# Kernel optimization log

Measured on AMD Instinct MI355X. Metric: run time of the kernel, lower is better.

Reference implementation:

```python
import jax, jax.numpy as jnp
import numpy as np

FILTER_K = 10      # per-class top-K support retention
TAU = 1.0          # temperature
SCALE = 20.0       # prototype logit scale
EPS = 1e-12


def _normalize(x, axis=-1):
    n = jnp.linalg.norm(x, axis=axis, keepdims=True)
    return x / jnp.maximum(n, EPS)


def _entropy(logits):
    p = jax.nn.softmax(logits, axis=1)
    return -(p * jax.nn.log_softmax(logits, axis=1)).sum(axis=1)


def _quantile(x, q):
    # linear-interpolation quantile (matches torch.quantile default)
    s = jnp.sort(x)
    n = x.shape[0]
    pos = q * (n - 1)
    lo = jnp.floor(pos).astype(jnp.int32)
    hi = jnp.minimum(lo + 1, n - 1)
    frac = pos - lo.astype(x.dtype)
    return s[lo] * (1.0 - frac) + s[hi] * frac


def setup_inputs() -> dict:
    key = jax.random.key(0)
    k1, k2, k3, k4, k5 = jax.random.split(key, 5)
    B, D, C = 65536, 512, 50
    feat = jax.random.normal(k1, (B, D), jnp.float32)
    logits_raw = jax.random.normal(k2, (B, C), jnp.float32)
    logits_aug = jax.random.normal(k3, (B, C), jnp.float32)
    W = jax.random.normal(k4, (C, D), jnp.float32) * 0.05  # classifier weight
    b = jax.random.normal(k5, (C,), jnp.float32) * 0.05    # classifier bias
    return {"feat": feat, "logits_raw": logits_raw, "logits_aug": logits_aug, "W": W, "b": b}


def reference(feat, logits_raw, logits_aug, W, b):
    C, D = W.shape
    # --- warmup memory initialized from classifier weights (as in __init__) ---
    wl = W @ W.T + b                       # (C, C)
    p0 = jax.nn.softmax(wl, axis=1)
    lab0 = jnp.argmax(wl, axis=1)          # (C,)
    ent0 = _entropy(wl)
    conf0 = p0.max(axis=1)

    # --- online batch stats ---
    logits = feat @ W.T + b                # (B, C)
    p = jax.nn.softmax(logits, axis=1)
    yhat = jnp.argmax(logits, axis=1)
    ent = _entropy(logits)
    pmax = p.max(axis=1)

    # dynamic entropy-quantile threshold (ent_thresh=None path)
    m = ent.mean()
    dyn_q = jnp.where(m >= 0.45, 0.25, jnp.where(m >= 0.38, 0.3, 0.4))
    thr = _quantile(ent, dyn_q)
    mask = ent <= thr
    # dual-view consistency gate
    mask &= jnp.argmax(logits_raw, axis=1) == jnp.argmax(logits_aug, axis=1)
    # confidence gate
    conf_thr = jnp.where(m >= 0.45, 0.72, 0.62)
    mask &= pmax >= conf_thr

    # --- grown support memory (warmup + accepted batch samples), static shape + valid mask ---
    supports = jnp.concatenate([W, feat], axis=0)          # (C+B, D)
    lab_idx = jnp.concatenate([lab0, yhat], axis=0)        # (C+B,)
    ents = jnp.concatenate([ent0, ent], axis=0)
    conf = jnp.concatenate([conf0, pmax], axis=0)
    valid = jnp.concatenate([jnp.ones((C,), bool), mask], axis=0)

    # --- per-class top-K lowest-entropy pruning (vectorized over classes) ---
    cls_mask = (lab_idx[None, :] == jnp.arange(C)[:, None]) & valid[None, :]  # (C, C+B)
    masked_ent = jnp.where(cls_mask, ents[None, :], jnp.inf)
    order = jnp.argsort(masked_ent, axis=1)
    ranks = jnp.argsort(order, axis=1)                     # rank of each entry within its class
    keep = (cls_mask & (ranks < FILTER_K)).any(axis=0)     # (C+B,)

    # --- confidence-weighted centroids + cosine-sim classification ---
    S = _normalize(supports)
    onehot = jax.nn.one_hot(lab_idx, C, dtype=supports.dtype)
    lab_w = onehot * jnp.maximum(conf, 1e-6)[:, None] * keep[:, None].astype(supports.dtype)
    denom = jnp.maximum(lab_w.sum(axis=0, keepdims=True), EPS)
    centroids = _normalize((lab_w / denom).T @ S)          # (C, D)
    sim = _normalize(feat) @ centroids.T                   # (B, C)
    return SCALE * sim / max(TAU, 1e-6)
```

## Files before the change

kernel.cpp:

```cpp
#include <hip/hip_runtime.h>
#include <math.h>

constexpr int BN = 65536;
constexpr int DK = 512;
constexpr int CN = 50;
constexpr int FILTK = 10;
constexpr int MB = 64;
constexpr int SELB = 64;
constexpr int CAP = 6144;
constexpr int ASTR = 132;

typedef __attribute__((ext_vector_type(8))) short short8;
typedef __attribute__((ext_vector_type(4))) float f4;

constexpr int W_SC     = 0;
constexpr int W_H1     = 64;
constexpr int W_H2LO   = 2112;
constexpr int W_H2HI   = 4160;
constexpr int W_H3LO   = 6208;
constexpr int W_H3HI   = 7232;
constexpr int ZERO_WORDS = 8256;
constexpr int W_WFH    = 8256;
constexpr int W_WFL    = W_WFH + 16384;
constexpr int W_CFH    = W_WFL + 16384;
constexpr int W_CFL    = W_CFH + 16384;
constexpr int W_ENT    = W_CFL + 16384;
constexpr int W_PMAX   = W_ENT  + BN;
constexpr int W_YHAT   = W_PMAX + BN;
constexpr int W_CONS   = W_YHAT + BN;
constexpr int W_NORM   = W_CONS + BN;
constexpr int W_LAB0   = W_NORM + BN;
constexpr int W_ENT0   = W_LAB0 + 64;
constexpr int W_CONF0  = W_ENT0 + 64;
constexpr int W_WNORM  = W_CONF0 + 64;
constexpr int LE_CAP   = BN + 64;
constexpr int W_LECLS  = W_WNORM + 64;
constexpr int W_LEENT  = W_LECLS  + LE_CAP;
constexpr int W_LECONF = W_LEENT  + LE_CAP;
constexpr int W_LEORD  = W_LECONF + LE_CAP;
constexpr int W_LESRC  = W_LEORD  + LE_CAP;

struct Scalars {
    float    sum_ent;
    float    mean;
    float    conf_thr;
    float    frac;
    int      klo;
    int      khi;
    unsigned prefix_lo;
    unsigned rank_lo;
    unsigned prefix_hi;
    unsigned rank_hi;
    float    thr;
    unsigned cnt;
    unsigned done1, done2, done3;
};

__device__ __forceinline__ unsigned fkey(float f) {
    unsigned u = __float_as_uint(f);
    return (u & 0x80000000u) ? ~u : (u | 0x80000000u);
}
__device__ __forceinline__ float funkey(unsigned u) {
    return (u & 0x80000000u) ? __uint_as_float(u & 0x7fffffffu) : __uint_as_float(~u);
}

__device__ __forceinline__ short bf16h(float x) {
    unsigned u = __float_as_uint(x);
    return (short)((u + 0x7fffu + ((u >> 16) & 1u)) >> 16);
}
__device__ __forceinline__ float bf16tof(short h) {
    return __uint_as_float(((unsigned)(unsigned short)h) << 16);
}
__device__ __forceinline__ void cvt8(const float* a, short8& h, short8& l) {
    #pragma unroll
    for (int j = 0; j < 8; j++) {
        short hh = bf16h(a[j]);
        h[j] = hh;
        l[j] = bf16h(a[j] - bf16tof(hh));
    }
}
__device__ __forceinline__ int fragidx(int ks, int n, int q, int j) {
    return ks * 2048 + (n >> 4) * 512 + ((n & 15) + 16 * q) * 8 + j;
}

__global__ void init_kernel(const float* __restrict__ W, const float* __restrict__ bias,
                            int* __restrict__ lab0, float* __restrict__ ent0,
                            float* __restrict__ conf0, float* __restrict__ wnorm,
                            unsigned* __restrict__ wsz,
                            short* __restrict__ wfh, short* __restrict__ wfl) {
    const int b = blockIdx.x, l = threadIdx.x;
    if (b >= 64) {
        for (int i = (b - 64) * 64 + l; i < ZERO_WORDS; i += 128) wsz[i] = 0u;
        return;
    }
    {
        int ks = l >> 2, q = l & 3;
        int dst = fragidx(ks, b, q, 0);
        if (b < CN) {
            const float* wp = W + b * DK + l * 8;
            f4 x = *(const f4*)wp, y = *(const f4*)(wp + 4);
            float a8[8] = {x[0], x[1], x[2], x[3], y[0], y[1], y[2], y[3]};
            short8 h, lo2; cvt8(a8, h, lo2);
            *(short8*)(wfh + dst) = h;
            *(short8*)(wfl + dst) = lo2;
        } else {
            short8 z;
            #pragma unroll
            for (int j = 0; j < 8; j++) z[j] = 0;
            *(short8*)(wfh + dst) = z;
            *(short8*)(wfl + dst) = z;
        }
    }
    if (b >= CN) return;

    __shared__ float wrow[DK];
    const int i = b;
    f4 v0 = *(const f4*)(W + i * DK + l * 4);
    f4 v1 = *(const f4*)(W + i * DK + 256 + l * 4);
    *(f4*)(wrow + l * 4) = v0;
    *(f4*)(wrow + 256 + l * 4) = v1;
    float sq = v0[0]*v0[0] + v0[1]*v0[1] + v0[2]*v0[2] + v0[3]*v0[3]
             + v1[0]*v1[0] + v1[1]*v1[1] + v1[2]*v1[2] + v1[3]*v1[3];
    #pragma unroll
    for (int m = 1; m < 64; m <<= 1) sq += __shfl_xor(sq, m);
    if (l == 0) wnorm[i] = sqrtf(sq);
    __syncthreads();

    float dot = -INFINITY;
    int   ai  = 0x7fffffff;
    if (l < CN) {
        const float* wj = W + l * DK;
        float d2 = 0.f;
        for (int d = 0; d < DK; d += 4) {
            f4 a = *(const f4*)(wrow + d);
            f4 b4 = *(const f4*)(wj + d);
            d2 = fmaf(a[0], b4[0], fmaf(a[1], b4[1], fmaf(a[2], b4[2], fmaf(a[3], b4[3], d2))));
        }
        dot = d2 + bias[l];
        ai  = l;
    }
    float mx = dot; int am = ai;
    #pragma unroll
    for (int m = 32; m >= 1; m >>= 1) {
        float o = __shfl_xor(mx, m); int oi = __shfl_xor(am, m);
        if (o > mx || (o == mx && oi < am)) { mx = o; am = oi; }
    }
    float e = 0.f, te = 0.f;
    if (l < CN) { e = expf(dot - mx); te = e * (dot - mx); }
    #pragma unroll
    for (int m = 1; m < 64; m <<= 1) { e += __shfl_xor(e, m); te += __shfl_xor(te, m); }
    if (l == 0) {
        lab0[i]  = am;
        ent0[i]  = logf(e) - te / e;
        conf0[i] = 1.f / e;
    }
}

template <int MODE>
__global__ __launch_bounds__(256) void gemm_kernel(
        const float* __restrict__ feat,
        const short* __restrict__ bfh, const short* __restrict__ bfl,
        const float* __restrict__ bias,
        float* __restrict__ ent, float* __restrict__ pmaxA,
        int* __restrict__ yhat, float* __restrict__ rnorm,
        const float* __restrict__ lraw, const float* __restrict__ laug,
        unsigned* __restrict__ consp, Scalars* sc, float* __restrict__ outp) {
    __shared__ float As[MB * ASTR];
    const int t = threadIdx.x;
    const int w = t >> 6, lane = t & 63, m = lane & 15, q = lane >> 4;
    const int rb = blockIdx.x * MB;
    const float* fbase = feat + (size_t)rb * DK;

    f4 acc[4];
    #pragma unroll
    for (int nt = 0; nt < 4; nt++) acc[nt] = (f4){0.f, 0.f, 0.f, 0.f};
    float sq = 0.f;

    const int scol = (t & 31) * 4;
    const int srow0 = t >> 5;

    for (int kc = 0; kc < 4; kc++) {
        if (kc) __syncthreads();
        #pragma unroll
        for (int r8 = 0; r8 < 8; r8++) {
            int row = r8 * 8 + srow0;
            f4 v = *(const f4*)(fbase + (size_t)row * DK + kc * 128 + scol);
            *(f4*)(&As[row * ASTR + scol]) = v;
        }
        __syncthreads();
        #pragma unroll
        for (int ks = 0; ks < 4; ks++) {
            const float* ap = &As[(w * 16 + m) * ASTR + ks * 32 + q * 8];
            f4 x = *(const f4*)ap;
            f4 y = *(const f4*)(ap + 4);
            float a8[8] = {x[0], x[1], x[2], x[3], y[0], y[1], y[2], y[3]};
            if (MODE == 0) {
                sq += x[0]*x[0] + x[1]*x[1] + x[2]*x[2] + x[3]*x[3]
                    + y[0]*y[0] + y[1]*y[1] + y[2]*y[2] + y[3]*y[3];
            }
            short8 ah, al;
            cvt8(a8, ah, al);
            const int ksg = kc * 4 + ks;
            short8 bh[4], bl[4];
            #pragma unroll
            for (int nt = 0; nt < 4; nt++) {
                int off = ksg * 2048 + nt * 512 + lane * 8;
                bh[nt] = *(const short8*)(bfh + off);
                bl[nt] = *(const short8*)(bfl + off);
            }
            #pragma unroll
            for (int nt = 0; nt < 4; nt++) {
                acc[nt] = __builtin_amdgcn_mfma_f32_16x16x32_bf16(ah, bh[nt], acc[nt], 0, 0, 0);
                acc[nt] = __builtin_amdgcn_mfma_f32_16x16x32_bf16(al, bh[nt], acc[nt], 0, 0, 0);
                acc[nt] = __builtin_amdgcn_mfma_f32_16x16x32_bf16(ah, bl[nt], acc[nt], 0, 0, 0);
            }
        }
    }

    if (MODE == 0) {
        float s = sq;
        s += __shfl_xor(s, 16);
        s += __shfl_xor(s, 32);
        if (q == 0) rnorm[rb + w * 16 + m] = sqrtf(s);
        __syncthreads();
        float* L = As;
        float bc[4];
        #pragma unroll
        for (int nt = 0; nt < 4; nt++) { int c = nt * 16 + m; bc[nt] = (c < CN) ? bias[c] : 0.f; }
        #pragma unroll
        for (int nt = 0; nt < 4; nt++)
            #pragma unroll
            for (int r = 0; r < 4; r++) {
                int row = w * 16 + q * 4 + r;
                L[row * 65 + nt * 16 + m] = acc[nt][r] + bc[nt];
            }
        __syncthreads();
        if (t < MB) {
            int grow = rb + t;
            const float* Lr = L + t * 65;
            float mx = Lr[0]; int am = 0;
            #pragma unroll 10
            for (int j = 1; j < CN; j++) { float v = Lr[j]; if (v > mx) { mx = v; am = j; } }
            float ssum = 0.f, tt = 0.f;
            for (int j = 0; j < CN; j++) {
                float d = Lr[j] - mx;
                float e = expf(d);
                ssum += e; tt += e * d;
            }
            float ev = logf(ssum) - tt / ssum;
            ent  [grow] = ev;
            pmaxA[grow] = 1.f / ssum;
            yhat [grow] = am;
            const float* rp  = lraw + (size_t)grow * CN;
            const float* apg = laug + (size_t)grow * CN;
            float m1 = rp[0];  int a1 = 0;
            float m2 = apg[0]; int a2 = 0;
            #pragma unroll 10
            for (int j = 1; j < CN; j++) {
                float v1 = rp[j];  if (v1 > m1) { m1 = v1; a1 = j; }
                float v2 = apg[j]; if (v2 > m2) { m2 = v2; a2 = j; }
            }
            consp[grow] = (a1 == a2) ? 1u : 0u;
            float es = ev;
            #pragma unroll
            for (int mk = 1; mk < 64; mk <<= 1) es += __shfl_xor(es, mk);
            if (t == 0) atomicAdd(&sc->sum_ent, es);
        }
    } else {
        #pragma unroll
        for (int r = 0; r < 4; r++) {
            int grow = rb + w * 16 + q * 4 + r;
            float s = 20.f / fmaxf(rnorm[grow], 1e-12f);
            #pragma unroll
            for (int nt = 0; nt < 4; nt++) {
                int c = nt * 16 + m;
                if (c < CN) outp[(size_t)grow * CN + c] = acc[nt][r] * s;
            }
        }
    }
}

__global__ __launch_bounds__(256) void sel1_kernel(const float* __restrict__ ent,
                                                   unsigned* __restrict__ H1, Scalars* sc) {
    __shared__ unsigned h[2048];
    __shared__ unsigned part[256];
    __shared__ int last;
    const int t = threadIdx.x;
    for (int b = t; b < 2048; b += 256) h[b] = 0u;
    __syncthreads();
    const int lo = blockIdx.x * (BN / SELB), hi = lo + (BN / SELB);
    for (int i = lo + t; i < hi; i += 256)
        atomicAdd(&h[fkey(ent[i]) >> 21], 1u);
    __syncthreads();
    for (int b = t; b < 2048; b += 256) if (h[b]) atomicAdd(&H1[b], h[b]);
    __threadfence();
    if (t == 0) last = (atomicAdd(&sc->done1, 1u) == SELB - 1) ? 1 : 0;
    __syncthreads();
    if (!last) return;

    for (int b = t; b < 2048; b += 256) h[b] = atomicAdd(&H1[b], 0u);
    __syncthreads();
    unsigned ps = 0;
    #pragma unroll
    for (int j = 0; j < 8; j++) ps += h[t * 8 + j];
    part[t] = ps;
    __syncthreads();
    if (t == 0) {
        float m = sc->sum_ent / (float)BN;
        sc->mean = m;
        float q = (m >= 0.45f) ? 0.25f : ((m >= 0.38f) ? 0.30f : 0.40f);
        sc->conf_thr = (m >= 0.45f) ? 0.72f : 0.62f;
        float pos = q * (float)(BN - 1);
        float flo = floorf(pos);
        sc->frac = pos - flo;
        int klo = (int)flo;
        int khi = klo + 1; if (khi > BN - 1) khi = BN - 1;
        sc->klo = klo; sc->khi = khi;
        for (int pass = 0; pass < 2; pass++) {
            unsigned k = (pass == 0) ? (unsigned)klo : (unsigned)khi;
            unsigned cum = 0; int c = 0;
            for (; c < 255; c++) { unsigned pc = part[c]; if (cum + pc > k) break; cum += pc; }
            int b = c * 8;
            for (; b < c * 8 + 7; b++) { unsigned hb = h[b]; if (cum + hb > k) break; cum += hb; }
            if (pass == 0) { sc->prefix_lo = (unsigned)b; sc->rank_lo = k - cum; }
            else           { sc->prefix_hi = (unsigned)b; sc->rank_hi = k - cum; }
        }
    }
}

__global__ __launch_bounds__(256) void sel2_kernel(const float* __restrict__ ent,
                                                   unsigned* __restrict__ HLO, unsigned* __restrict__ HHI,
                                                   Scalars* sc) {
    __shared__ unsigned hlo[2048], hhi[2048];
    __shared__ unsigned plo_s[256], phi_s[256];
    __shared__ int last;
    const int t = threadIdx.x;
    const unsigned plo = sc->prefix_lo, phi = sc->prefix_hi;
    for (int b = t; b < 2048; b += 256) { hlo[b] = 0u; hhi[b] = 0u; }
    __syncthreads();
    const int lo = blockIdx.x * (BN / SELB), hi = lo + (BN / SELB);
    for (int i = lo + t; i < hi; i += 256) {
        unsigned u = fkey(ent[i]);
        unsigned d1 = u >> 21, d2 = (u >> 10) & 2047u;
        if (d1 == plo) atomicAdd(&hlo[d2], 1u);
        if (d1 == phi) atomicAdd(&hhi[d2], 1u);
    }
    __syncthreads();
    for (int b = t; b < 2048; b += 256) {
        if (hlo[b]) atomicAdd(&HLO[b], hlo[b]);
        if (hhi[b]) atomicAdd(&HHI[b], hhi[b]);
    }
    __threadfence();
    if (t == 0) last = (atomicAdd(&sc->done2, 1u) == SELB - 1) ? 1 : 0;
    __syncthreads();
    if (!last) return;

    for (int b = t; b < 2048; b += 256) { hlo[b] = atomicAdd(&HLO[b], 0u); hhi[b] = atomicAdd(&HHI[b], 0u); }
    __syncthreads();
    unsigned pl = 0, ph = 0;
    #pragma unroll
    for (int j = 0; j < 8; j++) { pl += hlo[t * 8 + j]; ph += hhi[t * 8 + j]; }
    plo_s[t] = pl; phi_s[t] = ph;
    __syncthreads();
    if (t == 0) {
        {
            unsigned k = sc->rank_lo, cum = 0; int c = 0;
            for (; c < 255; c++) { unsigned pc = plo_s[c]; if (cum + pc > k) break; cum += pc; }
            int b = c * 8;
            for (; b < c * 8 + 7; b++) { unsigned hb = hlo[b]; if (cum + hb > k) break; cum += hb; }
            sc->prefix_lo = (plo << 11) | (unsigned)b; sc->rank_lo = k - cum;
        }
        {
            unsigned k = sc->rank_hi, cum = 0; int c = 0;
            for (; c < 255; c++) { unsigned pc = phi_s[c]; if (cum + pc > k) break; cum += pc; }
            int b = c * 8;
            for (; b < c * 8 + 7; b++) { unsigned hb = hhi[b]; if (cum + hb > k) break; cum += hb; }
            sc->prefix_hi = (phi << 11) | (unsigned)b; sc->rank_hi = k - cum;
        }
    }
}

__global__ __launch_bounds__(256) void sel3_kernel(const float* __restrict__ ent,
                                                   unsigned* __restrict__ HLO, unsigned* __restrict__ HHI,
                                                   Scalars* sc) {
    __shared__ unsigned hlo[1024], hhi[1024];
    __shared__ unsigned plo_s[256], phi_s[256];
    __shared__ int last;
    const int t = threadIdx.x;
    const unsigned plo = sc->prefix_lo, phi = sc->prefix_hi;
    for (int b = t; b < 1024; b += 256) { hlo[b] = 0u; hhi[b] = 0u; }
    __syncthreads();
    const int lo = blockIdx.x * (BN / SELB), hi = lo + (BN / SELB);
    for (int i = lo + t; i < hi; i += 256) {
        unsigned u = fkey(ent[i]);
        unsigned p22 = u >> 10, d3 = u & 1023u;
        if (p22 == plo) atomicAdd(&hlo[d3], 1u);
        if (p22 == phi) atomicAdd(&hhi[d3], 1u);
    }
    __syncthreads();
    for (int b = t; b < 1024; b += 256) {
        if (hlo[b]) atomicAdd(&HLO[b], hlo[b]);
        if (hhi[b]) atomicAdd(&HHI[b], hhi[b]);
    }
    __threadfence();
    if (t == 0) last = (atomicAdd(&sc->done3, 1u) == SELB - 1) ? 1 : 0;
    __syncthreads();
    if (!last) return;

    for (int b = t; b < 1024; b += 256) { hlo[b] = atomicAdd(&HLO[b], 0u); hhi[b] = atomicAdd(&HHI[b], 0u); }
    __syncthreads();
    unsigned pl = 0, ph = 0;
    #pragma unroll
    for (int j = 0; j < 4; j++) { pl += hlo[t * 4 + j]; ph += hhi[t * 4 + j]; }
    plo_s[t] = pl; phi_s[t] = ph;
    __syncthreads();
    if (t == 0) {
        float vlo, vhi;
        {
            unsigned k = sc->rank_lo, cum = 0; int c = 0;
            for (; c < 255; c++) { unsigned pc = plo_s[c]; if (cum + pc > k) break; cum += pc; }
            int b = c * 4;
            for (; b < c * 4 + 3; b++) { unsigned hb = hlo[b]; if (cum + hb > k) break; cum += hb; }
            vlo = funkey((plo << 10) | (unsigned)b);
        }
        {
            unsigned k = sc->rank_hi, cum = 0; int c = 0;
            for (; c < 255; c++) { unsigned pc = phi_s[c]; if (cum + pc > k) break; cum += pc; }
            int b = c * 4;
            for (; b < c * 4 + 3; b++) { unsigned hb = hhi[b]; if (cum + hb > k) break; cum += hb; }
            vhi = funkey((phi << 10) | (unsigned)b);
        }
        sc->thr = vlo * (1.f - sc->frac) + vhi * sc->frac;
    }
}

__global__ __launch_bounds__(256) void compact_kernel(
        const float* __restrict__ ent, const float* __restrict__ pmaxA,
        const int* __restrict__ yhat, const unsigned* __restrict__ cons,
        const int* __restrict__ lab0, const float* __restrict__ ent0,
        const float* __restrict__ conf0, Scalars* sc,
        int* le_cls, float* le_ent, float* le_conf, int* le_ord, int* le_src) {
    int i = blockIdx.x * blockDim.x + threadIdx.x;
    if (i < CN) {
        le_cls[i] = lab0[i]; le_ent[i] = ent0[i]; le_conf[i] = conf0[i];
        le_ord[i] = i; le_src[i] = i;
    }
    if (i >= BN) return;
    bool m = (ent[i] <= sc->thr) && (cons[i] != 0u) && (pmaxA[i] >= sc->conf_thr);
    if (m) {
        int pos = (int)atomicAdd(&sc->cnt, 1u);
        int e = CN + pos;
        le_cls[e] = yhat[i]; le_ent[e] = ent[i]; le_conf[e] = pmaxA[i];
        le_ord[e] = CN + i;  le_src[e] = i;
    }
}

__global__ __launch_bounds__(256) void tail2_kernel(
        const Scalars* sc, const int* __restrict__ le_cls,
        const float* __restrict__ le_ent, const float* __restrict__ le_conf,
        const int* __restrict__ le_ord, const int* __restrict__ le_src,
        const float* __restrict__ W, const float* __restrict__ feat,
        const float* __restrict__ wnorm, const float* __restrict__ rnorm,
        short* __restrict__ cfh, short* __restrict__ cfl) {
    const int c = blockIdx.x, t = threadIdx.x;
    if (c >= CN) {
        for (int idx = t; idx < 512; idx += 256) {
            int ks = idx >> 5, rem = idx & 31, qq = rem >> 3, jj = rem & 7;
            int dst = fragidx(ks, c, qq, jj);
            cfh[dst] = 0; cfl[dst] = 0;
        }
        return;
    }
    __shared__ float sent[CAP];
    __shared__ int   sord[CAP];
    __shared__ float sconf[CAP];
    __shared__ int   ssrc[CAP];
    __shared__ float wk[CAP];
    __shared__ float accv[DK];
    __shared__ float red[4];
    __shared__ int   mc_s;
    if (t == 0) mc_s = 0;
    for (int d = t; d < DK; d += 256) accv[d] = 0.f;
    __syncthreads();
    const int M = CN + (int)sc->cnt;
    for (int e = t; e < M; e += 256) {
        if (le_cls[e] == c) {
            int i = atomicAdd(&mc_s, 1);
            if (i < CAP) { sent[i] = le_ent[e]; sord[i] = le_ord[e]; sconf[i] = le_conf[e]; ssrc[i] = le_src[e]; }
        }
    }
    __syncthreads();
    int mc = min(mc_s, CAP);
    for (int i = t; i < mc; i += 256) {
        float v = sent[i]; int o = sord[i]; int r = 0;
        for (int j = 0; j < mc && r < FILTK; j++)
            if (sent[j] < v || (sent[j] == v && sord[j] < o)) r++;
        wk[i] = (r < FILTK) ? fmaxf(sconf[i], 1e-6f) : 0.f;
    }
    __syncthreads();
    for (int i = 0; i < mc; i++) {
        float wgt = wk[i];
        if (wgt <= 0.f) continue;
        int src = ssrc[i];
        bool warm = sord[i] < CN;
        const float* rowp = warm ? (W + src * DK) : (feat + (size_t)src * DK);
        float nr = warm ? wnorm[src] : rnorm[src];
        float k = wgt / fmaxf(nr, 1e-12f);
        for (int d = t; d < DK; d += 256) accv[d] += k * rowp[d];
    }
    __syncthreads();
    float s = 0.f;
    for (int d = t; d < DK; d += 256) { float v = accv[d]; s = fmaf(v, v, s); }
    #pragma unroll
    for (int mk = 1; mk < 64; mk <<= 1) s += __shfl_xor(s, mk);
    if ((t & 63) == 0) red[t >> 6] = s;
    __syncthreads();
    float inv = 1.f / fmaxf(sqrtf(red[0] + red[1] + red[2] + red[3]), 1e-12f);
    for (int k = t; k < DK; k += 256) {
        float v = accv[k] * inv;
        short hh = bf16h(v);
        short ll = bf16h(v - bf16tof(hh));
        int ks = k >> 5, kk = k & 31, qq = kk >> 3, jj = kk & 7;
        int dst = fragidx(ks, c, qq, jj);
        cfh[dst] = hh; cfl[dst] = ll;
    }
}

extern "C" void kernel_launch(void* const* d_in, const int* in_sizes, int n_in,
                              void* d_out, int out_size, void* d_ws, size_t ws_size,
                              hipStream_t stream) {
    const float* feat = (const float*)d_in[0];
    const float* lraw = (const float*)d_in[1];
    const float* laug = (const float*)d_in[2];
    const float* W    = (const float*)d_in[3];
    const float* bias = (const float*)d_in[4];
    float* out = (float*)d_out;

    unsigned* wsw    = (unsigned*)d_ws;
    Scalars*  sc     = (Scalars*)(wsw + W_SC);
    unsigned* H1     = wsw + W_H1;
    unsigned* H2LO   = wsw + W_H2LO;
    unsigned* H2HI   = wsw + W_H2HI;
    unsigned* H3LO   = wsw + W_H3LO;
    unsigned* H3HI   = wsw + W_H3HI;
    short*    wfh    = (short*)(wsw + W_WFH);
    short*    wfl    = (short*)(wsw + W_WFL);
    short*    cfh    = (short*)(wsw + W_CFH);
    short*    cfl    = (short*)(wsw + W_CFL);
    float*    ent    = (float*)(wsw + W_ENT);
    float*    pmaxA  = (float*)(wsw + W_PMAX);
    int*      yhat   = (int*)(wsw + W_YHAT);
    unsigned* cons   = wsw + W_CONS;
    float*    rnorm  = (float*)(wsw + W_NORM);
    int*      lab0   = (int*)(wsw + W_LAB0);
    float*    ent0   = (float*)(wsw + W_ENT0);
    float*    conf0  = (float*)(wsw + W_CONF0);
    float*    wnorm  = (float*)(wsw + W_WNORM);
    int*      le_cls = (int*)(wsw + W_LECLS);
    float*    le_ent = (float*)(wsw + W_LEENT);
    float*    le_conf= (float*)(wsw + W_LECONF);
    int*      le_ord = (int*)(wsw + W_LEORD);
    int*      le_src = (int*)(wsw + W_LESRC);

    init_kernel<<<66, 64, 0, stream>>>(W, bias, lab0, ent0, conf0, wnorm, wsw, wfh, wfl);
    gemm_kernel<0><<<BN / MB, 256, 0, stream>>>(feat, wfh, wfl, bias, ent, pmaxA, yhat, rnorm,
                                                lraw, laug, cons, sc, nullptr);
    sel1_kernel<<<SELB, 256, 0, stream>>>(ent, H1, sc);
    sel2_kernel<<<SELB, 256, 0, stream>>>(ent, H2LO, H2HI, sc);
    sel3_kernel<<<SELB, 256, 0, stream>>>(ent, H3LO, H3HI, sc);
    compact_kernel<<<BN / 256, 256, 0, stream>>>(ent, pmaxA, yhat, cons, lab0, ent0, conf0, sc,
                                                 le_cls, le_ent, le_conf, le_ord, le_src);
    tail2_kernel<<<64, 256, 0, stream>>>(sc, le_cls, le_ent, le_conf, le_ord, le_src,
                                         W, feat, wnorm, rnorm, cfh, cfl);
    gemm_kernel<1><<<BN / MB, 256, 0, stream>>>(feat, cfh, cfl, nullptr, nullptr, nullptr, nullptr, rnorm,
                                                nullptr, nullptr, nullptr, sc, out);
}
```

Baseline: 357.5 us.

## Double-buffer per-wave LDS tiles in GEMM, drop block barriers, simplify bf16 split

Each wave now stages only its own 16 feature rows into a private double-buffered LDS region. The next k-chunk is prefetched into registers while the current chunk is consumed, which removes the block-wide __syncthreads between chunks. The B fragments for a whole k-chunk are also loaded up front. Separately, the bf16 hi/lo split switches from round-to-nearest-even to a simpler round-half-up, and launch bounds request 2 blocks per CU. The costs are much higher register pressure (bh/bl arrays of 32 short8 plus 8 staged f4), a larger LDS footprint, and slightly different rounding of the split.

```diff
diff --git a/kernel.cpp b/kernel.cpp
--- a/kernel.cpp
+++ b/kernel.cpp
@@ -8,7 +8,8 @@
 constexpr int MB = 64;
 constexpr int SELB = 64;
 constexpr int CAP = 6144;
-constexpr int ASTR = 132;
+constexpr int WSTR = 132;
+constexpr int WBUF = 16 * WSTR;
 
 typedef __attribute__((ext_vector_type(8))) short short8;
 typedef __attribute__((ext_vector_type(4))) float f4;
@@ -64,20 +65,21 @@
     return (u & 0x80000000u) ? __uint_as_float(u & 0x7fffffffu) : __uint_as_float(~u);
 }
 
+__device__ __forceinline__ void cvt8(const float* a, short8& h, short8& l) {
+    #pragma unroll
+    for (int j = 0; j < 8; j++) {
+        unsigned u = __float_as_uint(a[j]);
+        unsigned r = (u + 0x8000u) & 0xffff0000u;
+        float lo_f = a[j] - __uint_as_float(r);
+        h[j] = (short)(r >> 16);
+        l[j] = (short)((__float_as_uint(lo_f) + 0x8000u) >> 16);
+    }
+}
 __device__ __forceinline__ short bf16h(float x) {
-    unsigned u = __float_as_uint(x);
-    return (short)((u + 0x7fffu + ((u >> 16) & 1u)) >> 16);
+    return (short)((__float_as_uint(x) + 0x8000u) >> 16);
 }
 __device__ __forceinline__ float bf16tof(short h) {
     return __uint_as_float(((unsigned)(unsigned short)h) << 16);
-}
-__device__ __forceinline__ void cvt8(const float* a, short8& h, short8& l) {
-    #pragma unroll
-    for (int j = 0; j < 8; j++) {
-        short hh = bf16h(a[j]);
-        h[j] = hh;
-        l[j] = bf16h(a[j] - bf16tof(hh));
-    }
 }
 __device__ __forceinline__ int fragidx(int ks, int n, int q, int j) {
     return ks * 2048 + (n >> 4) * 512 + ((n & 15) + 16 * q) * 8 + j;
@@ -157,7 +159,7 @@
 }
 
 template <int MODE>
-__global__ __launch_bounds__(256) void gemm_kernel(
+__global__ __launch_bounds__(256, 2) void gemm_kernel(
         const float* __restrict__ feat,
         const short* __restrict__ bfh, const short* __restrict__ bfl,
         const float* __restrict__ bias,
@@ -165,55 +167,73 @@
         int* __restrict__ yhat, float* __restrict__ rnorm,
         const float* __restrict__ lraw, const float* __restrict__ laug,
         unsigned* __restrict__ consp, Scalars* sc, float* __restrict__ outp) {
-    __shared__ float As[MB * ASTR];
+    __shared__ float As[4 * 2 * WBUF];
     const int t = threadIdx.x;
     const int w = t >> 6, lane = t & 63, m = lane & 15, q = lane >> 4;
     const int rb = blockIdx.x * MB;
-    const float* fbase = feat + (size_t)rb * DK;
+    const int wr0 = rb + w * 16;
+    float* myLDS = As + w * (2 * WBUF);
+
+    const int sr  = lane >> 5;
+    const int sc4 = lane & 31;
 
     f4 acc[4];
     #pragma unroll
     for (int nt = 0; nt < 4; nt++) acc[nt] = (f4){0.f, 0.f, 0.f, 0.f};
     float sq = 0.f;
 
-    const int scol = (t & 31) * 4;
-    const int srow0 = t >> 5;
+    {
+        f4 stg[8];
+        #pragma unroll
+        for (int r8 = 0; r8 < 8; r8++)
+            stg[r8] = *(const f4*)(feat + (size_t)(wr0 + r8 * 2 + sr) * DK + sc4 * 4);
+        #pragma unroll
+        for (int r8 = 0; r8 < 8; r8++)
+            *(f4*)(myLDS + (r8 * 2 + sr) * WSTR + sc4 * 4) = stg[r8];
+    }
 
     for (int kc = 0; kc < 4; kc++) {
-        if (kc) __syncthreads();
-        #pragma unroll
-        for (int r8 = 0; r8 < 8; r8++) {
-            int row = r8 * 8 + srow0;
-            f4 v = *(const f4*)(fbase + (size_t)row * DK + kc * 128 + scol);
-            *(f4*)(&As[row * ASTR + scol]) = v;
-        }
-        __syncthreads();
+        const int cur = kc & 1;
+        short8 bh[4][4], bl[4][4];
         #pragma unroll
         for (int ks = 0; ks < 4; ks++) {
-            const float* ap = &As[(w * 16 + m) * ASTR + ks * 32 + q * 8];
+            const int ksg = kc * 4 + ks;
+            #pragma unroll
+            for (int nt = 0; nt < 4; nt++) {
+                const int off = ksg * 2048 + nt * 512 + lane * 8;
+                bh[ks][nt] = *(const short8*)(bfh + off);
+                bl[ks][nt] = *(const short8*)(bfl + off);
+            }
+        }
+        f4 stg[8];
+        if (kc < 3) {
+            #pragma unroll
+            for (int r8 = 0; r8 < 8; r8++)
+                stg[r8] = *(const f4*)(feat + (size_t)(wr0 + r8 * 2 + sr) * DK + (kc + 1) * 128 + sc4 * 4);
+        }
+        #pragma unroll
+        for (int ks = 0; ks < 4; ks++) {
+            const float* ap = myLDS + cur * WBUF + m * WSTR + ks * 32 + q * 8;
             f4 x = *(const f4*)ap;
             f4 y = *(const f4*)(ap + 4);
-            float a8[8] = {x[0], x[1], x[2], x[3], y[0], y[1], y[2], y[3]};
             if (MODE == 0) {
                 sq += x[0]*x[0] + x[1]*x[1] + x[2]*x[2] + x[3]*x[3]
                     + y[0]*y[0] + y[1]*y[1] + y[2]*y[2] + y[3]*y[3];
             }
+            float a8[8] = {x[0], x[1], x[2], x[3], y[0], y[1], y[2], y[3]};
             short8 ah, al;
             cvt8(a8, ah, al);
-            const int ksg = kc * 4 + ks;
-            short8 bh[4], bl[4];
             #pragma unroll
             for (int nt = 0; nt < 4; nt++) {
-                int off = ksg * 2048 + nt * 512 + lane * 8;
-                bh[nt] = *(const short8*)(bfh + off);
-                bl[nt] = *(const short8*)(bfl + off);
-            }
-            #pragma unroll
-            for (int nt = 0; nt < 4; nt++) {
-                acc[nt] = __builtin_amdgcn_mfma_f32_16x16x32_bf16(ah, bh[nt], acc[nt], 0, 0, 0);
-                acc[nt] = __builtin_amdgcn_mfma_f32_16x16x32_bf16(al, bh[nt], acc[nt], 0, 0, 0);
-                acc[nt] = __builtin_amdgcn_mfma_f32_16x16x32_bf16(ah, bl[nt], acc[nt], 0, 0, 0);
-            }
+                acc[nt] = __builtin_amdgcn_mfma_f32_16x16x32_bf16(ah, bh[ks][nt], acc[nt], 0, 0, 0);
+                acc[nt] = __builtin_amdgcn_mfma_f32_16x16x32_bf16(al, bh[ks][nt], acc[nt], 0, 0, 0);
+                acc[nt] = __builtin_amdgcn_mfma_f32_16x16x32_bf16(ah, bl[ks][nt], acc[nt], 0, 0, 0);
+            }
+        }
+        if (kc < 3) {
+            #pragma unroll
+            for (int r8 = 0; r8 < 8; r8++)
+                *(f4*)(myLDS + (cur ^ 1) * WBUF + (r8 * 2 + sr) * WSTR + sc4 * 4) = stg[r8];
         }
     }
 
@@ -221,7 +241,7 @@
         float s = sq;
         s += __shfl_xor(s, 16);
         s += __shfl_xor(s, 32);
-        if (q == 0) rnorm[rb + w * 16 + m] = sqrtf(s);
+        if (q == 0) rnorm[wr0 + m] = sqrtf(s);
         __syncthreads();
         float* L = As;
         float bc[4];
@@ -269,7 +289,7 @@
     } else {
         #pragma unroll
         for (int r = 0; r < 4; r++) {
-            int grow = rb + w * 16 + q * 4 + r;
+            int grow = wr0 + q * 4 + r;
             float s = 20.f / fmaxf(rnorm[grow], 1e-12f);
             #pragma unroll
             for (int nt = 0; nt < 4; nt++) {
```

New measurement: 361.9 us. No clear change (+1.2%).
